# Performance work log

Hardware: AMD Instinct MI355X
Metric: run time of the kernel (lower is better)

The kernel has to match this reference:

```python
import jax, jax.numpy as jnp
import numpy as np
from jax.scipy.special import logsumexp

N, D = 8192, 128
NUM_CLASSES = 100
M_MARGIN = 0.25
GAMMA = 256.0


def setup_inputs() -> dict:
    key = jax.random.key(0)
    k1, k2 = jax.random.split(key)
    features = jax.random.normal(k1, (N, D), dtype=jnp.float32)
    labels = jax.random.randint(k2, (N,), 0, NUM_CLASSES, dtype=jnp.int64)
    return {"features": features, "labels": labels}


def reference(features, labels):
    m, gamma = M_MARGIN, GAMMA
    # L2-normalize rows (torch F.normalize with eps=1e-12)
    norm = jnp.maximum(jnp.linalg.norm(features, axis=1, keepdims=True), 1e-12)
    f = features / norm
    sim = f @ f.T  # [N, N] cosine similarities

    eq = labels[:, None] == labels[None, :]
    pos_mask = jnp.triu(eq, k=1)            # same-label pairs, i < j
    neg_mask = jnp.triu(jnp.logical_not(eq), k=1)  # diff-label pairs, i < j

    sim_d = jax.lax.stop_gradient(sim)
    ap = jnp.maximum(-sim_d + 1.0 + m, 0.0)
    an = jnp.maximum(sim_d + m, 0.0)

    delta_p = 1.0 - m
    delta_n = m
    neg_inf = jnp.float32(-jnp.inf)
    # Masked logits: excluded entries -> -inf so masked logsumexp matches
    # torch's boolean-compaction + logsumexp exactly.
    logit_p = jnp.where(pos_mask, -ap * (sim - delta_p) * gamma, neg_inf)
    logit_n = jnp.where(neg_mask, an * (sim - delta_n) * gamma, neg_inf)

    loss = jax.nn.softplus(logsumexp(logit_n) + logsumexp(logit_p))
    return loss
```

## Files before the change

kernel.cpp:

```cpp
#include <hip/hip_runtime.h>
#include <hip/hip_bf16.h>
#include <cstdint>

#define N_PTS 8192
#define DIM 128

typedef __attribute__((ext_vector_type(8))) __bf16 bf16x8;
typedef __attribute__((ext_vector_type(4))) float f32x4;

#define KC2 369.3299304675746f
#define KC1 -738.6598609351493f
#define KC0 346.2468098133512f
#define KCN0 -23.083120654223414f
#define NEGH -1e30f
#define LN2F 0.6931471805599453f

__device__ __forceinline__ unsigned short f2bf(float x) {
  unsigned int u = __float_as_uint(x);
  unsigned int r = (u + 0x7FFFu + ((u >> 16) & 1u)) >> 16;
  return (unsigned short)r;
}

__global__ __launch_bounds__(256) void normalize_kernel(const float* __restrict__ feat,
                                                        unsigned short* __restrict__ fb) {
  const int row = blockIdx.x * 4 + (threadIdx.x >> 6);
  const int lane = threadIdx.x & 63;
  const float2 v = *(const float2*)(feat + row * DIM + lane * 2);
  float ss = v.x * v.x + v.y * v.y;
#pragma unroll
  for (int o = 32; o > 0; o >>= 1) ss += __shfl_xor(ss, o);
  const float inv = 1.0f / fmaxf(sqrtf(ss), 1e-12f);
  const unsigned int pack =
      (unsigned int)f2bf(v.x * inv) | ((unsigned int)f2bf(v.y * inv) << 16);
  *(unsigned int*)(fb + row * DIM + lane * 2) = pack;
}

__global__ __launch_bounds__(256) void pair_kernel(const unsigned short* __restrict__ f,
                                                   const int* __restrict__ labels,
                                                   float4* __restrict__ partials) {
  const int tI = blockIdx.y, tJ = blockIdx.x;
  const int slot = tI * 64 + tJ;
  if (tJ < tI) {
    if (threadIdx.x == 0) partials[slot] = make_float4(NEGH, 0.f, NEGH, 0.f);
    return;
  }

  __shared__ __align__(16) unsigned short sA[128 * 32];
  __shared__ __align__(16) unsigned short sB[128 * 32];
  __shared__ float redbuf[8];

  const int t = threadIdx.x;
  const int lane = t & 63, wave = t >> 6;
  const int wr = (wave >> 1) * 64, wc = (wave & 1) * 64;
  const int rsel = lane & 15, ksel = (lane >> 4) * 8;

  f32x4 acc[4][4];
#pragma unroll
  for (int a = 0; a < 4; ++a)
#pragma unroll
    for (int b = 0; b < 4; ++b) acc[a][b] = (f32x4){0.f, 0.f, 0.f, 0.f};

  const int rowA0 = tI * 128, rowB0 = tJ * 128;

  for (int kk = 0; kk < 4; ++kk) {
    const int k0 = kk * 32;
    if (kk) __syncthreads();
#pragma unroll
    for (int c0 = 0; c0 < 2; ++c0) {
      const int c = t + c0 * 256;
      const int r = c >> 2, e = (c & 3) * 8;
      *(uint4*)(&sA[r * 32 + e]) = *(const uint4*)(f + (rowA0 + r) * DIM + k0 + e);
      *(uint4*)(&sB[r * 32 + e]) = *(const uint4*)(f + (rowB0 + r) * DIM + k0 + e);
    }
    __syncthreads();
    bf16x8 fa[4], fbv[4];
#pragma unroll
    for (int x = 0; x < 4; ++x) {
      fa[x] = *(const bf16x8*)(&sA[(wr + x * 16 + rsel) * 32 + ksel]);
      fbv[x] = *(const bf16x8*)(&sB[(wc + x * 16 + rsel) * 32 + ksel]);
    }
#pragma unroll
    for (int tm = 0; tm < 4; ++tm)
#pragma unroll
      for (int tn = 0; tn < 4; ++tn)
        acc[tm][tn] =
            __builtin_amdgcn_mfma_f32_16x16x32_bf16(fa[tm], fbv[tn], acc[tm][tn], 0, 0, 0);
  }

  const int ibase = tI * 128 + wr + (lane >> 4) * 4;
  const int jbase = tJ * 128 + wc + rsel;
  int li[4][4], lj[4];
#pragma unroll
  for (int tn = 0; tn < 4; ++tn) lj[tn] = labels[jbase + tn * 16];
#pragma unroll
  for (int tm = 0; tm < 4; ++tm)
#pragma unroll
    for (int r = 0; r < 4; ++r) li[tm][r] = labels[ibase + tm * 16 + r];

  float mp = NEGH, mn = NEGH;
  if (tI != tJ) {
#pragma unroll
    for (int tm = 0; tm < 4; ++tm)
#pragma unroll
      for (int tn = 0; tn < 4; ++tn)
#pragma unroll
        for (int r = 0; r < 4; ++r) {
          const float s = acc[tm][tn][r];
          const float w = s * KC2;
          const float lp = fmaf(s, w + KC1, KC0);
          const float ln = (s > -0.25f) ? fmaf(s, w, KCN0) : 0.f;
          const bool eq = (li[tm][r] == lj[tn]);
          acc[tm][tn][r] = eq ? lp : ln;
          mp = fmaxf(mp, eq ? lp : NEGH);
          mn = fmaxf(mn, eq ? NEGH : ln);
        }
  } else {
#pragma unroll
    for (int tm = 0; tm < 4; ++tm)
#pragma unroll
      for (int tn = 0; tn < 4; ++tn) {
        const int d = (jbase + tn * 16) - (ibase + tm * 16);
#pragma unroll
        for (int r = 0; r < 4; ++r) {
          const float s = acc[tm][tn][r];
          const float w = s * KC2;
          const float lp = fmaf(s, w + KC1, KC0);
          const float ln = (s > -0.25f) ? fmaf(s, w, KCN0) : 0.f;
          const bool eq = (li[tm][r] == lj[tn]);
          const bool valid = d > r;
          float u = eq ? lp : ln;
          u = valid ? u : NEGH;
          acc[tm][tn][r] = u;
          mp = fmaxf(mp, (eq && valid) ? lp : NEGH);
          mn = fmaxf(mn, (!eq && valid) ? ln : NEGH);
        }
      }
  }
#pragma unroll
  for (int o = 32; o > 0; o >>= 1) {
    mp = fmaxf(mp, __shfl_xor(mp, o));
    mn = fmaxf(mn, __shfl_xor(mn, o));
  }
  if (lane == 0) { redbuf[wave] = mp; redbuf[4 + wave] = mn; }
  __syncthreads();
  const float Mp = fmaxf(fmaxf(fmaxf(redbuf[0], redbuf[1]), fmaxf(redbuf[2], redbuf[3])), -1e28f);
  const float Mn = fmaxf(fmaxf(fmaxf(redbuf[4], redbuf[5]), fmaxf(redbuf[6], redbuf[7])), -1e28f);
  __syncthreads();

  float sp = 0.f, sn = 0.f;
#pragma unroll
  for (int tm = 0; tm < 4; ++tm)
#pragma unroll
    for (int tn = 0; tn < 4; ++tn)
#pragma unroll
      for (int r = 0; r < 4; ++r) {
        const bool eq = (li[tm][r] == lj[tn]);
        const float e = __builtin_amdgcn_exp2f(acc[tm][tn][r] - (eq ? Mp : Mn));
        sp += eq ? e : 0.f;
        sn += eq ? 0.f : e;
      }
#pragma unroll
  for (int o = 32; o > 0; o >>= 1) {
    sp += __shfl_xor(sp, o);
    sn += __shfl_xor(sn, o);
  }
  if (lane == 0) { redbuf[wave] = sp; redbuf[4 + wave] = sn; }
  __syncthreads();
  if (t == 0) {
    partials[slot] = make_float4(Mp, redbuf[0] + redbuf[1] + redbuf[2] + redbuf[3],
                                 Mn, redbuf[4] + redbuf[5] + redbuf[6] + redbuf[7]);
  }
}

__global__ __launch_bounds__(256) void finalize_kernel(const float4* __restrict__ partials,
                                                       float* __restrict__ out) {
  const int t = threadIdx.x;
  float mp = NEGH, sp = 0.f, mn = NEGH, sn = 0.f;
  for (int i = t; i < 4096; i += 256) {
    const float4 p = partials[i];
    {
      const float m = fmaxf(mp, p.x);
      sp = sp * __builtin_amdgcn_exp2f(mp - m) + p.y * __builtin_amdgcn_exp2f(p.x - m);
      mp = m;
    }
    {
      const float m = fmaxf(mn, p.z);
      sn = sn * __builtin_amdgcn_exp2f(mn - m) + p.w * __builtin_amdgcn_exp2f(p.z - m);
      mn = m;
    }
  }
  __shared__ float smp[256], ssp[256], smn[256], ssn[256];
  smp[t] = mp; ssp[t] = sp; smn[t] = mn; ssn[t] = sn;
  __syncthreads();
  for (int off = 128; off > 0; off >>= 1) {
    if (t < off) {
      {
        const float m2 = smp[t + off], s2 = ssp[t + off];
        const float m = fmaxf(smp[t], m2);
        ssp[t] = ssp[t] * __builtin_amdgcn_exp2f(smp[t] - m) + s2 * __builtin_amdgcn_exp2f(m2 - m);
        smp[t] = m;
      }
      {
        const float m2 = smn[t + off], s2 = ssn[t + off];
        const float m = fmaxf(smn[t], m2);
        ssn[t] = ssn[t] * __builtin_amdgcn_exp2f(smn[t] - m) + s2 * __builtin_amdgcn_exp2f(m2 - m);
        smn[t] = m;
      }
    }
    __syncthreads();
  }
  if (t == 0) {
    const float lsep = (smp[0] + __builtin_amdgcn_logf(ssp[0])) * LN2F;
    const float lsen = (smn[0] + __builtin_amdgcn_logf(ssn[0])) * LN2F;
    const float x = lsep + lsen;
    out[0] = fmaxf(x, 0.f) + log1pf(__expf(-fabsf(x)));
  }
}

extern "C" void kernel_launch(void* const* d_in, const int* in_sizes, int n_in,
                              void* d_out, int out_size, void* d_ws, size_t ws_size,
                              hipStream_t stream) {
  const float* feat = (const float*)d_in[0];
  const int* labels = (const int*)d_in[1];
  float* out = (float*)d_out;

  unsigned short* fb = (unsigned short*)d_ws;
  float4* partials = (float4*)((char*)d_ws + (size_t)N_PTS * DIM * 2);

  normalize_kernel<<<N_PTS / 4, 256, 0, stream>>>(feat, fb);
  dim3 grid(64, 64);
  pair_kernel<<<grid, 256, 0, stream>>>(fb, labels, partials);
  finalize_kernel<<<1, 256, 0, stream>>>(partials, out);
}
```

Before: 108.2 us.

## Triangular grid, async LDS double-buffering, byte labels, fused last-block finalize

Launches only the upper-triangular tile blocks, mapping a linear block id to (tI,tJ) instead of running and early-exiting lower-triangle blocks. The K loop now uses global_load_lds straight into double-buffered, XOR-swizzled shared memory so the next K slice loads while the current one runs on MFMA. Labels are packed to bytes in the normalize kernel, and the finalize kernel is folded into pair_kernel through an atomic counter, with the last block doing the reduction. This removes a launch and idle blocks, at the cost of an atomic, threadfences and extra occupancy pressure.

```diff
diff --git a/kernel.cpp b/kernel.cpp
--- a/kernel.cpp
+++ b/kernel.cpp
@@ -4,9 +4,7 @@
 
 #define N_PTS 8192
 #define DIM 128
-
-typedef __attribute__((ext_vector_type(8))) __bf16 bf16x8;
-typedef __attribute__((ext_vector_type(4))) float f32x4;
+#define NBLK 2080
 
 #define KC2 369.3299304675746f
 #define KC1 -738.6598609351493f
@@ -15,14 +13,29 @@
 #define NEGH -1e30f
 #define LN2F 0.6931471805599453f
 
+typedef __attribute__((ext_vector_type(8))) __bf16 bf16x8;
+typedef __attribute__((ext_vector_type(4))) float f32x4;
+
 __device__ __forceinline__ unsigned short f2bf(float x) {
   unsigned int u = __float_as_uint(x);
   unsigned int r = (u + 0x7FFFu + ((u >> 16) & 1u)) >> 16;
   return (unsigned short)r;
 }
 
+__device__ __forceinline__ void gll16(const unsigned short* g, unsigned short* l) {
+  __builtin_amdgcn_global_load_lds(
+      (const __attribute__((address_space(1))) unsigned int*)g,
+      (__attribute__((address_space(3))) unsigned int*)l, 16, 0, 0);
+}
+
 __global__ __launch_bounds__(256) void normalize_kernel(const float* __restrict__ feat,
-                                                        unsigned short* __restrict__ fb) {
+                                                        const int* __restrict__ labels,
+                                                        unsigned short* __restrict__ fb,
+                                                        unsigned char* __restrict__ lab8,
+                                                        unsigned int* __restrict__ cnt) {
+  const int gid = blockIdx.x * 256 + threadIdx.x;
+  if (gid == 0) *cnt = 0u;
+  if (gid < N_PTS) lab8[gid] = (unsigned char)labels[gid];
   const int row = blockIdx.x * 4 + (threadIdx.x >> 6);
   const int lane = threadIdx.x & 63;
   const float2 v = *(const float2*)(feat + row * DIM + lane * 2);
@@ -35,24 +48,39 @@
   *(unsigned int*)(fb + row * DIM + lane * 2) = pack;
 }
 
-__global__ __launch_bounds__(256) void pair_kernel(const unsigned short* __restrict__ f,
-                                                   const int* __restrict__ labels,
-                                                   float4* __restrict__ partials) {
-  const int tI = blockIdx.y, tJ = blockIdx.x;
-  const int slot = tI * 64 + tJ;
-  if (tJ < tI) {
-    if (threadIdx.x == 0) partials[slot] = make_float4(NEGH, 0.f, NEGH, 0.f);
-    return;
-  }
-
-  __shared__ __align__(16) unsigned short sA[128 * 32];
-  __shared__ __align__(16) unsigned short sB[128 * 32];
-  __shared__ float redbuf[8];
+__global__ __launch_bounds__(256, 5) void pair_kernel(const unsigned short* __restrict__ f,
+                                                      const unsigned char* __restrict__ lab8,
+                                                      float4* __restrict__ partials,
+                                                      unsigned int* __restrict__ cnt,
+                                                      float* __restrict__ out) {
+  __shared__ __align__(16) unsigned short sA[2][4096];
+  __shared__ __align__(16) unsigned short sB[2][4096];
+
+  const int bid = blockIdx.x;
+  int tI = (int)((129.0f - sqrtf(16641.0f - 8.0f * (float)bid)) * 0.5f);
+  while (tI * (129 - tI) / 2 > bid) --tI;
+  while ((tI + 1) * (128 - tI) / 2 <= bid) ++tI;
+  const int tJ = tI + (bid - tI * (129 - tI) / 2);
 
   const int t = threadIdx.x;
   const int lane = t & 63, wave = t >> 6;
   const int wr = (wave >> 1) * 64, wc = (wave & 1) * 64;
-  const int rsel = lane & 15, ksel = (lane >> 4) * 8;
+  const int rsel = lane & 15;
+  const int qcol = ((lane >> 4) ^ ((rsel >> 1) & 3)) * 8;
+
+  const int r0 = t >> 2;
+  const int q0 = (t & 3) ^ ((r0 >> 1) & 3);
+  const int eoff = r0 * DIM + q0 * 8;
+  const unsigned short* gA = f + tI * 128 * DIM + eoff;
+  const unsigned short* gB = f + tJ * 128 * DIM + eoff;
+
+#define STAGE(buf, k0)                                   \
+  do {                                                   \
+    gll16(gA + (k0), &sA[buf][t * 8]);                   \
+    gll16(gA + (k0) + 64 * DIM, &sA[buf][2048 + t * 8]); \
+    gll16(gB + (k0), &sB[buf][t * 8]);                   \
+    gll16(gB + (k0) + 64 * DIM, &sB[buf][2048 + t * 8]); \
+  } while (0)
 
   f32x4 acc[4][4];
 #pragma unroll
@@ -60,24 +88,16 @@
 #pragma unroll
     for (int b = 0; b < 4; ++b) acc[a][b] = (f32x4){0.f, 0.f, 0.f, 0.f};
 
-  const int rowA0 = tI * 128, rowB0 = tJ * 128;
-
+  STAGE(0, 0);
+  __syncthreads();
   for (int kk = 0; kk < 4; ++kk) {
-    const int k0 = kk * 32;
-    if (kk) __syncthreads();
-#pragma unroll
-    for (int c0 = 0; c0 < 2; ++c0) {
-      const int c = t + c0 * 256;
-      const int r = c >> 2, e = (c & 3) * 8;
-      *(uint4*)(&sA[r * 32 + e]) = *(const uint4*)(f + (rowA0 + r) * DIM + k0 + e);
-      *(uint4*)(&sB[r * 32 + e]) = *(const uint4*)(f + (rowB0 + r) * DIM + k0 + e);
-    }
-    __syncthreads();
+    const int cur = kk & 1;
+    if (kk < 3) STAGE(cur ^ 1, (kk + 1) * 32);
     bf16x8 fa[4], fbv[4];
 #pragma unroll
     for (int x = 0; x < 4; ++x) {
-      fa[x] = *(const bf16x8*)(&sA[(wr + x * 16 + rsel) * 32 + ksel]);
-      fbv[x] = *(const bf16x8*)(&sB[(wc + x * 16 + rsel) * 32 + ksel]);
+      fa[x] = *(const bf16x8*)(&sA[cur][(wr + x * 16 + rsel) * 32 + qcol]);
+      fbv[x] = *(const bf16x8*)(&sB[cur][(wc + x * 16 + rsel) * 32 + qcol]);
     }
 #pragma unroll
     for (int tm = 0; tm < 4; ++tm)
@@ -85,17 +105,19 @@
       for (int tn = 0; tn < 4; ++tn)
         acc[tm][tn] =
             __builtin_amdgcn_mfma_f32_16x16x32_bf16(fa[tm], fbv[tn], acc[tm][tn], 0, 0, 0);
-  }
-
+    __syncthreads();
+  }
+#undef STAGE
+
+  float* redbuf = (float*)&sA[0][0];
   const int ibase = tI * 128 + wr + (lane >> 4) * 4;
   const int jbase = tJ * 128 + wc + rsel;
-  int li[4][4], lj[4];
-#pragma unroll
-  for (int tn = 0; tn < 4; ++tn) lj[tn] = labels[jbase + tn * 16];
+  unsigned int liPack[4], lj[4];
+#pragma unroll
+  for (int tn = 0; tn < 4; ++tn) lj[tn] = lab8[jbase + tn * 16];
 #pragma unroll
   for (int tm = 0; tm < 4; ++tm)
-#pragma unroll
-    for (int r = 0; r < 4; ++r) li[tm][r] = labels[ibase + tm * 16 + r];
+    liPack[tm] = *(const unsigned int*)(lab8 + ibase + tm * 16);
 
   float mp = NEGH, mn = NEGH;
   if (tI != tJ) {
@@ -109,7 +131,7 @@
           const float w = s * KC2;
           const float lp = fmaf(s, w + KC1, KC0);
           const float ln = (s > -0.25f) ? fmaf(s, w, KCN0) : 0.f;
-          const bool eq = (li[tm][r] == lj[tn]);
+          const bool eq = (((liPack[tm] >> (r * 8)) & 0xFFu) == lj[tn]);
           acc[tm][tn][r] = eq ? lp : ln;
           mp = fmaxf(mp, eq ? lp : NEGH);
           mn = fmaxf(mn, eq ? NEGH : ln);
@@ -126,7 +148,7 @@
           const float w = s * KC2;
           const float lp = fmaf(s, w + KC1, KC0);
           const float ln = (s > -0.25f) ? fmaf(s, w, KCN0) : 0.f;
-          const bool eq = (li[tm][r] == lj[tn]);
+          const bool eq = (((liPack[tm] >> (r * 8)) & 0xFFu) == lj[tn]);
           const bool valid = d > r;
           float u = eq ? lp : ln;
           u = valid ? u : NEGH;
@@ -154,7 +176,7 @@
     for (int tn = 0; tn < 4; ++tn)
 #pragma unroll
       for (int r = 0; r < 4; ++r) {
-        const bool eq = (li[tm][r] == lj[tn]);
+        const bool eq = (((liPack[tm] >> (r * 8)) & 0xFFu) == lj[tn]);
         const float e = __builtin_amdgcn_exp2f(acc[tm][tn][r] - (eq ? Mp : Mn));
         sp += eq ? e : 0.f;
         sn += eq ? 0.f : e;
@@ -166,31 +188,38 @@
   }
   if (lane == 0) { redbuf[wave] = sp; redbuf[4 + wave] = sn; }
   __syncthreads();
+
+  unsigned int* flag = (unsigned int*)&sB[0][0];
   if (t == 0) {
-    partials[slot] = make_float4(Mp, redbuf[0] + redbuf[1] + redbuf[2] + redbuf[3],
-                                 Mn, redbuf[4] + redbuf[5] + redbuf[6] + redbuf[7]);
-  }
-}
-
-__global__ __launch_bounds__(256) void finalize_kernel(const float4* __restrict__ partials,
-                                                       float* __restrict__ out) {
-  const int t = threadIdx.x;
-  float mp = NEGH, sp = 0.f, mn = NEGH, sn = 0.f;
-  for (int i = t; i < 4096; i += 256) {
+    partials[bid] = make_float4(Mp, redbuf[0] + redbuf[1] + redbuf[2] + redbuf[3],
+                                Mn, redbuf[4] + redbuf[5] + redbuf[6] + redbuf[7]);
+    __threadfence();
+    const unsigned int old = atomicAdd(cnt, 1u);
+    __threadfence();
+    flag[0] = (old == NBLK - 1) ? 1u : 0u;
+  }
+  __syncthreads();
+  if (flag[0] == 0u) return;
+
+  float fmp = NEGH, fsp = 0.f, fmn = NEGH, fsn = 0.f;
+  for (int i = t; i < NBLK; i += 256) {
     const float4 p = partials[i];
     {
-      const float m = fmaxf(mp, p.x);
-      sp = sp * __builtin_amdgcn_exp2f(mp - m) + p.y * __builtin_amdgcn_exp2f(p.x - m);
-      mp = m;
+      const float m = fmaxf(fmp, p.x);
+      fsp = fsp * __builtin_amdgcn_exp2f(fmp - m) + p.y * __builtin_amdgcn_exp2f(p.x - m);
+      fmp = m;
     }
     {
-      const float m = fmaxf(mn, p.z);
-      sn = sn * __builtin_amdgcn_exp2f(mn - m) + p.w * __builtin_amdgcn_exp2f(p.z - m);
-      mn = m;
-    }
-  }
-  __shared__ float smp[256], ssp[256], smn[256], ssn[256];
-  smp[t] = mp; ssp[t] = sp; smn[t] = mn; ssn[t] = sn;
+      const float m = fmaxf(fmn, p.z);
+      fsn = fsn * __builtin_amdgcn_exp2f(fmn - m) + p.w * __builtin_amdgcn_exp2f(p.z - m);
+      fmn = m;
+    }
+  }
+  float* smp = (float*)&sA[0][0];
+  float* ssp = smp + 256;
+  float* smn = smp + 512;
+  float* ssn = smp + 768;
+  smp[t] = fmp; ssp[t] = fsp; smn[t] = fmn; ssn[t] = fsn;
   __syncthreads();
   for (int off = 128; off > 0; off >>= 1) {
     if (t < off) {
@@ -225,10 +254,11 @@
   float* out = (float*)d_out;
 
   unsigned short* fb = (unsigned short*)d_ws;
-  float4* partials = (float4*)((char*)d_ws + (size_t)N_PTS * DIM * 2);
-
-  normalize_kernel<<<N_PTS / 4, 256, 0, stream>>>(feat, fb);
-  dim3 grid(64, 64);
-  pair_kernel<<<grid, 256, 0, stream>>>(fb, labels, partials);
-  finalize_kernel<<<1, 256, 0, stream>>>(partials, out);
-}
+  char* base = (char*)d_ws + (size_t)N_PTS * DIM * 2;
+  float4* partials = (float4*)base;
+  unsigned int* cnt = (unsigned int*)(base + 33280);
+  unsigned char* lab8 = (unsigned char*)(base + 33296);
+
+  normalize_kernel<<<N_PTS / 4, 256, 0, stream>>>(feat, labels, fb, lab8, cnt);
+  pair_kernel<<<NBLK, 256, 0, stream>>>(fb, lab8, partials, cnt, out);
+}
```

Measured after the change: 224.4 us. +107.4%, slower.
